# Optimization experiments

Measured on AMD Instinct MI355X. Metric: run time of the kernel, lower is better.

The kernel has to match this reference:

```python
import jax, jax.numpy as jnp
import numpy as np

LN_EPS = 1e-5


def setup_inputs() -> dict:
    key = jax.random.key(0)
    ks = jax.random.split(key, 8)
    dim = 256
    b, n3 = 8, 6144  # seq dim holds 3 concatenated token streams of n=2048 each
    s = 0.02
    return {
        "x": jax.random.normal(ks[0], (b, n3, dim), jnp.float32),
        "ln_g": jnp.ones((dim,), jnp.float32),
        "ln_b": jnp.zeros((dim,), jnp.float32),
        "Wq": jax.random.normal(ks[1], (dim, dim), jnp.float32) * s,
        "bq": jax.random.normal(ks[2], (dim,), jnp.float32) * s,
        "Wk": jax.random.normal(ks[3], (dim, dim), jnp.float32) * s,
        "bk": jax.random.normal(ks[4], (dim,), jnp.float32) * s,
        "Wv": jax.random.normal(ks[5], (dim, dim), jnp.float32) * s,
        "bv": jax.random.normal(ks[6], (dim,), jnp.float32) * s,
        "Wo": jax.random.normal(ks[7], (dim, dim), jnp.float32) * s,
        "bo": jnp.zeros((dim,), jnp.float32),
        "heads": 8,
    }


def reference(x, ln_g, ln_b, Wq, bq, Wk, bk, Wv, bv, Wo, bo, heads):
    dim = x.shape[-1]
    scale = dim ** (-0.5)  # NOTE: full dim, as in the original module
    d = dim // heads

    def cross_attn(xcat):
        # LayerNorm over last dim (applied to concatenated [2b, n, dim])
        mu = jnp.mean(xcat, axis=-1, keepdims=True)
        var = jnp.mean(jnp.square(xcat - mu), axis=-1, keepdims=True)
        xn = (xcat - mu) * jax.lax.rsqrt(var + LN_EPS) * ln_g + ln_b
        x1, x2 = jnp.split(xn, 2, axis=0)  # queries from stream 1, kv from stream 2
        q = x1 @ Wq.T + bq
        k = x2 @ Wk.T + bk
        v = x2 @ Wv.T + bv
        b_, n_ = q.shape[0], q.shape[1]
        q = q.reshape(b_, n_, heads, d).transpose(0, 2, 1, 3)  # b h n d
        k = k.reshape(b_, n_, heads, d).transpose(0, 2, 1, 3)
        v = v.reshape(b_, n_, heads, d).transpose(0, 2, 1, 3)
        dots = jnp.einsum('bhid,bhjd->bhij', q, k) * scale
        attn = jax.nn.softmax(dots, axis=-1)
        out = jnp.einsum('bhij,bhjd->bhid', attn, v)
        out = out.transpose(0, 2, 1, 3).reshape(b_, n_, dim)
        return out @ Wo.T + bo  # dropout is identity in eval

    x_origin, x_emap, x_lbp = jnp.split(x, 3, axis=1)
    out_oe = cross_attn(jnp.concatenate((x_origin, x_emap), axis=0))
    out_ol = cross_attn(jnp.concatenate((x_origin, x_lbp), axis=0))
    return out_oe + out_ol
```

## Files before the change

### kernel.cpp

```cpp
#include <hip/hip_runtime.h>
#include <hip/hip_bf16.h>
#include <math.h>

#define LN_EPS 1e-5f
#define QSCALE 0.09016844005556021f

typedef __attribute__((ext_vector_type(8))) short short8;
typedef __attribute__((ext_vector_type(4))) short short4v;
typedef __attribute__((ext_vector_type(4))) float f32x4;

__device__ inline ushort f2bf(float f) {
  __hip_bfloat16 h = __float2bfloat16(f);
  return *reinterpret_cast<ushort*>(&h);
}

__device__ inline uint pk2bf(float a, float b) {
  uint ua = __float_as_uint(a) + 0x8000u;
  uint ub = __float_as_uint(b) + 0x8000u;
  return __builtin_amdgcn_perm(ub, ua, 0x07060302u);
}


__global__ __launch_bounds__(256) void ln_wcast_kernel(
    const float* __restrict__ x, const float* __restrict__ lng,
    const float* __restrict__ lnb,
    const float* __restrict__ Wq, const float* __restrict__ Wk,
    const float* __restrict__ Wv, const float* __restrict__ Wo,
    ushort* __restrict__ xn, ushort* __restrict__ wbf) {
  if (blockIdx.x < 256) {
    int t = blockIdx.x * 256 + threadIdx.x;
    int e0 = t * 4;
    int m = e0 >> 16, off = e0 & 65535;
    const float* src = (m == 0) ? Wq : (m == 1) ? Wk : (m == 2) ? Wv : Wo;
    float4 v = *(const float4*)(src + off);
    ushort4 o;
    o.x = f2bf(v.x); o.y = f2bf(v.y); o.z = f2bf(v.z); o.w = f2bf(v.w);
    *(ushort4*)(wbf + m * 65536 + off) = o;
    return;
  }
  int w = threadIdx.x >> 6;
  int lane = threadIdx.x & 63;
  size_t token = (size_t)(blockIdx.x - 256) * 4 + w;
  float4 v = *(const float4*)(x + token * 256 + lane * 4);
  float s  = v.x + v.y + v.z + v.w;
  float s2 = v.x * v.x + v.y * v.y + v.z * v.z + v.w * v.w;
#pragma unroll
  for (int off = 32; off >= 1; off >>= 1) {
    s  += __shfl_xor(s, off, 64);
    s2 += __shfl_xor(s2, off, 64);
  }
  float mu  = s * (1.0f / 256.0f);
  float var = s2 * (1.0f / 256.0f) - mu * mu;
  float rs  = rsqrtf(var + LN_EPS);
  float4 g = *(const float4*)(lng + lane * 4);
  float4 bb = *(const float4*)(lnb + lane * 4);
  ushort4 o;
  o.x = f2bf((v.x - mu) * rs * g.x + bb.x);
  o.y = f2bf((v.y - mu) * rs * g.y + bb.y);
  o.z = f2bf((v.z - mu) * rs * g.z + bb.z);
  o.w = f2bf((v.w - mu) * rs * g.w + bb.w);
  *(ushort4*)(xn + token * 256 + lane * 4) = o;
}

__global__ __launch_bounds__(256) void proj_kernel(
    const ushort* __restrict__ xn,
    const ushort* __restrict__ wq, const ushort* __restrict__ wk,
    const ushort* __restrict__ wv,
    const float* __restrict__ bq, const float* __restrict__ bk,
    const float* __restrict__ bv,
    ushort* __restrict__ qb, ushort* __restrict__ keb, ushort* __restrict__ vTe,
    ushort* __restrict__ klb, ushort* __restrict__ vTl) {
  int z = blockIdx.z;
  int tid = threadIdx.x;
  int w = tid >> 6, lane = tid & 63;
  int n = lane & 15, quad = lane >> 4;
  int cbase = blockIdx.y * 128 + w * 32;
  int b = (blockIdx.x * 128) >> 11;
  int r0 = (blockIdx.x * 128) & 2047;

  if (z == 0) {
    const ushort* xbase = xn + ((size_t)b * 6144 + r0) * 256;
    short8 wf[2][8];
#pragma unroll
    for (int ct = 0; ct < 2; ++ct)
#pragma unroll
      for (int kc = 0; kc < 8; ++kc)
        wf[ct][kc] = *(const short8*)(wq + (size_t)(cbase + ct * 16 + n) * 256 + kc * 32 + quad * 8);
    float4 bt[2];
    bt[0] = *(const float4*)(bq + cbase + quad * 4);
    bt[1] = *(const float4*)(bq + cbase + 16 + quad * 4);

    short8 xfA[8], xfB[8];
#pragma unroll
    for (int kc = 0; kc < 8; ++kc)
      xfA[kc] = *(const short8*)(xbase + (size_t)n * 256 + kc * 32 + quad * 8);

#pragma unroll
    for (int tt = 0; tt < 8; ++tt) {
      const short8* cur = (tt & 1) ? xfB : xfA;
      short8* nxt = (tt & 1) ? xfA : xfB;
      if (tt < 7) {
#pragma unroll
        for (int kc = 0; kc < 8; ++kc)
          nxt[kc] = *(const short8*)(xbase + (size_t)((tt + 1) * 16 + n) * 256 + kc * 32 + quad * 8);
      }
      f32x4 acc[2] = {{0.f, 0.f, 0.f, 0.f}, {0.f, 0.f, 0.f, 0.f}};
#pragma unroll
      for (int ct = 0; ct < 2; ++ct)
#pragma unroll
        for (int kc = 0; kc < 8; ++kc)
          acc[ct] = __builtin_amdgcn_mfma_f32_16x16x32_bf16(wf[ct][kc], cur[kc], acc[ct], 0, 0, 0);
      int n2 = r0 + tt * 16 + n;
#pragma unroll
      for (int ct = 0; ct < 2; ++ct) {
        int c = cbase + ct * 16 + quad * 4;
        int h = c >> 5, d = c & 31;
        float* bp = (float*)&bt[ct];
        ushort4 st;
        st.x = f2bf((acc[ct][0] + bp[0]) * QSCALE);
        st.y = f2bf((acc[ct][1] + bp[1]) * QSCALE);
        st.z = f2bf((acc[ct][2] + bp[2]) * QSCALE);
        st.w = f2bf((acc[ct][3] + bp[3]) * QSCALE);
        *(ushort4*)(qb + (((size_t)(b * 8 + h) * 2048) + n2) * 32 + d) = st;
      }
    }
  } else {
    int s = z;
    ushort* kout = (z == 1) ? keb : klb;
    ushort* vout = (z == 1) ? vTe : vTl;
    const ushort* xbase = xn + ((size_t)b * 6144 + s * 2048 + r0) * 256;
    short8 wfk[2][8], wfv[2][8];
#pragma unroll
    for (int ct = 0; ct < 2; ++ct)
#pragma unroll
      for (int kc = 0; kc < 8; ++kc) {
        wfk[ct][kc] = *(const short8*)(wk + (size_t)(cbase + ct * 16 + n) * 256 + kc * 32 + quad * 8);
        wfv[ct][kc] = *(const short8*)(wv + (size_t)(cbase + ct * 16 + n) * 256 + kc * 32 + quad * 8);
      }
    float4 btk[2];
    btk[0] = *(const float4*)(bk + cbase + quad * 4);
    btk[1] = *(const float4*)(bk + cbase + 16 + quad * 4);
    float bsv[2] = {bv[cbase + n], bv[cbase + 16 + n]};

    short8 xfA[8], xfB[8];
#pragma unroll
    for (int kc = 0; kc < 8; ++kc)
      xfA[kc] = *(const short8*)(xbase + (size_t)n * 256 + kc * 32 + quad * 8);

#pragma unroll
    for (int tt = 0; tt < 8; ++tt) {
      const short8* cur = (tt & 1) ? xfB : xfA;
      short8* nxt = (tt & 1) ? xfA : xfB;
      if (tt < 7) {
#pragma unroll
        for (int kc = 0; kc < 8; ++kc)
          nxt[kc] = *(const short8*)(xbase + (size_t)((tt + 1) * 16 + n) * 256 + kc * 32 + quad * 8);
      }
      f32x4 ack[2] = {{0.f, 0.f, 0.f, 0.f}, {0.f, 0.f, 0.f, 0.f}};
      f32x4 acv[2] = {{0.f, 0.f, 0.f, 0.f}, {0.f, 0.f, 0.f, 0.f}};
#pragma unroll
      for (int ct = 0; ct < 2; ++ct)
#pragma unroll
        for (int kc = 0; kc < 8; ++kc) {
          ack[ct] = __builtin_amdgcn_mfma_f32_16x16x32_bf16(wfk[ct][kc], cur[kc], ack[ct], 0, 0, 0);
          acv[ct] = __builtin_amdgcn_mfma_f32_16x16x32_bf16(cur[kc], wfv[ct][kc], acv[ct], 0, 0, 0);
        }
      int n2 = r0 + tt * 16 + n;
#pragma unroll
      for (int ct = 0; ct < 2; ++ct) {
        int c = cbase + ct * 16 + quad * 4;
        int h = c >> 5, d = c & 31;
        float* bp = (float*)&btk[ct];
        ushort4 st;
        st.x = f2bf(ack[ct][0] + bp[0]);
        st.y = f2bf(ack[ct][1] + bp[1]);
        st.z = f2bf(ack[ct][2] + bp[2]);
        st.w = f2bf(ack[ct][3] + bp[3]);
        *(ushort4*)(kout + (((size_t)(b * 8 + h) * 2048) + n2) * 32 + d) = st;
      }
      int tq = r0 + tt * 16 + quad * 4;
      int tile = tq >> 6;
      int t4 = (tq >> 4) & 3;
      int qp = (tq >> 2) & 3;
#pragma unroll
      for (int ct = 0; ct < 2; ++ct) {
        int c = cbase + ct * 16 + n;
        int h = c >> 5, d = c & 31;
        int dh = d >> 4, np = d & 15;
        ushort4 st;
        st.x = f2bf(acv[ct][0] + bsv[ct]);
        st.y = f2bf(acv[ct][1] + bsv[ct]);
        st.z = f2bf(acv[ct][2] + bsv[ct]);
        st.w = f2bf(acv[ct][3] + bsv[ct]);
        *(ushort4*)(vout + (size_t)(b * 8 + h) * 65536
                    + (size_t)((((tile * 2 + dh) * 4 + t4) * 64 + qp * 16 + np) * 4)) = st;
      }
    }
  }
}

__global__ __launch_bounds__(256, 3) void attn_kernel(
    const ushort* __restrict__ q,
    const ushort* __restrict__ ke, const ushort* __restrict__ vTe,
    const ushort* __restrict__ kl, const ushort* __restrict__ vTl,
    ushort* __restrict__ osum) {
  int tid = threadIdx.x;
  int w = tid >> 6, lane = tid & 63;
  int n = lane & 15, quad = lane >> 4;

  union { uint2 u; short4v s; } one_u;
  one_u.u.x = 0x3F803F80u; one_u.u.y = 0x3F803F80u;
  const short4v vone = one_u.s;

  int L = blockIdx.y * 8 + blockIdx.x;
  int xcd = L & 7, idx = L >> 3;
  int bh = (idx & 7) * 8 + xcd;
  int q0 = (idx >> 3) * 128;
  int qbase = q0 + w * 32;

  short8 qfrag[2];
#pragma unroll
  for (int gq = 0; gq < 2; ++gq)
    qfrag[gq] = *(const short8*)(q + ((size_t)bh * 2048 + qbase + gq * 16 + n) * 32 + quad * 8);

  f32x4 outv[2][2];
#pragma unroll
  for (int gq = 0; gq < 2; ++gq)
#pragma unroll
    for (int dh = 0; dh < 2; ++dh) outv[gq][dh] = (f32x4){0.f, 0.f, 0.f, 0.f};

  for (int s = 0; s < 2; ++s) {
    const ushort* K  = (s == 0 ? ke : kl) + (size_t)bh * 2048 * 32;
    const ushort* VT = (s == 0 ? vTe : vTl) + (size_t)bh * 65536;
    f32x4 lacc[2];
    f32x4 oacc[2][2];
#pragma unroll
    for (int gq = 0; gq < 2; ++gq) {
      lacc[gq] = (f32x4){0.f, 0.f, 0.f, 0.f};
#pragma unroll
      for (int dh = 0; dh < 2; ++dh) oacc[gq][dh] = (f32x4){0.f, 0.f, 0.f, 0.f};
    }

    short8 kfc[4], kfn[4];
    short4v vfc[2][4], vfn[2][4];
#pragma unroll
    for (int t4 = 0; t4 < 4; ++t4)
      kfc[t4] = *(const short8*)(K + (size_t)(t4 * 16 + n) * 32 + quad * 8);
#pragma unroll
    for (int dh = 0; dh < 2; ++dh)
#pragma unroll
      for (int t4 = 0; t4 < 4; ++t4)
        vfc[dh][t4] = *(const short4v*)(VT + (dh * 4 + t4) * 256 + lane * 4);

    for (int jt = 0; jt < 32; ++jt) {
      if (jt < 31) {
        size_t tb = (size_t)(jt + 1) * 2048;
#pragma unroll
        for (int t4 = 0; t4 < 4; ++t4)
          kfn[t4] = *(const short8*)(K + tb + (size_t)(t4 * 16 + n) * 32 + quad * 8);
#pragma unroll
        for (int dh = 0; dh < 2; ++dh)
#pragma unroll
          for (int t4 = 0; t4 < 4; ++t4)
            vfn[dh][t4] = *(const short4v*)(VT + tb + (dh * 4 + t4) * 256 + lane * 4);
      }
#pragma unroll
      for (int gq = 0; gq < 2; ++gq) {
        f32x4 sacc[4];
#pragma unroll
        for (int t4 = 0; t4 < 4; ++t4) {
          f32x4 z = {0.f, 0.f, 0.f, 0.f};
          sacc[t4] = __builtin_amdgcn_mfma_f32_16x16x32_bf16(kfc[t4], qfrag[gq], z, 0, 0, 0);
        }
        short4v pf[4];
#pragma unroll
        for (int t4 = 0; t4 < 4; ++t4) {
          float p0 = __builtin_amdgcn_exp2f(sacc[t4][0]);
          float p1 = __builtin_amdgcn_exp2f(sacc[t4][1]);
          float p2 = __builtin_amdgcn_exp2f(sacc[t4][2]);
          float p3 = __builtin_amdgcn_exp2f(sacc[t4][3]);
          union { uint2 u; short4v s4; } cv;
          cv.u.x = pk2bf(p0, p1);
          cv.u.y = pk2bf(p2, p3);
          pf[t4] = cv.s4;
        }
#pragma unroll
        for (int t4 = 0; t4 < 4; ++t4) {
          oacc[gq][0] = __builtin_amdgcn_mfma_f32_16x16x16bf16_1k(
              pf[t4], vfc[0][t4], oacc[gq][0], 0, 0, 0);
          oacc[gq][1] = __builtin_amdgcn_mfma_f32_16x16x16bf16_1k(
              pf[t4], vfc[1][t4], oacc[gq][1], 0, 0, 0);
          lacc[gq] = __builtin_amdgcn_mfma_f32_16x16x16bf16_1k(
              pf[t4], vone, lacc[gq], 0, 0, 0);
        }
      }
#pragma unroll
      for (int t4 = 0; t4 < 4; ++t4) kfc[t4] = kfn[t4];
#pragma unroll
      for (int dh = 0; dh < 2; ++dh)
#pragma unroll
        for (int t4 = 0; t4 < 4; ++t4) vfc[dh][t4] = vfn[dh][t4];
    }
#pragma unroll
    for (int gq = 0; gq < 2; ++gq) {
      f32x4 inv;
#pragma unroll
      for (int r = 0; r < 4; ++r) inv[r] = __builtin_amdgcn_rcpf(lacc[gq][r]);
#pragma unroll
      for (int dh = 0; dh < 2; ++dh)
        outv[gq][dh] += oacc[gq][dh] * inv;
    }
  }

  int b = bh >> 3, h = bh & 7;
#pragma unroll
  for (int gq = 0; gq < 2; ++gq)
#pragma unroll
    for (int dh = 0; dh < 2; ++dh) {
      f32x4 v = outv[gq][dh];
#pragma unroll
      for (int r = 0; r < 4; ++r) {
        size_t row = (size_t)b * 2048 + qbase + gq * 16 + quad * 4 + r;
        osum[row * 256 + h * 32 + dh * 16 + n] = f2bf(v[r]);
      }
    }
}

__global__ __launch_bounds__(256) void outproj_kernel(
    const ushort* __restrict__ osum, const ushort* __restrict__ wo,
    const float* __restrict__ bo, float* __restrict__ out) {
  int tid = threadIdx.x;
  int w = tid >> 6, lane = tid & 63;
  int n = lane & 15, quad = lane >> 4;
  int cbase = blockIdx.y * 128 + w * 32;

  short8 wfrag[2][8];
#pragma unroll
  for (int ct = 0; ct < 2; ++ct)
#pragma unroll
    for (int kc = 0; kc < 8; ++kc)
      wfrag[ct][kc] = *(const short8*)(wo + (size_t)(cbase + ct * 16 + n) * 256 + kc * 32 + quad * 8);
  float4 bt[2];
  bt[0] = *(const float4*)(bo + cbase + quad * 4);
  bt[1] = *(const float4*)(bo + cbase + 16 + quad * 4);

  const ushort* abase = osum + (size_t)(blockIdx.x * 128) * 256;
  short8 xfA[8], xfB[8];
#pragma unroll
  for (int kc = 0; kc < 8; ++kc)
    xfA[kc] = *(const short8*)(abase + (size_t)n * 256 + kc * 32 + quad * 8);

#pragma unroll
  for (int tt = 0; tt < 8; ++tt) {
    const short8* cur = (tt & 1) ? xfB : xfA;
    short8* nxt = (tt & 1) ? xfA : xfB;
    if (tt < 7) {
#pragma unroll
      for (int kc = 0; kc < 8; ++kc)
        nxt[kc] = *(const short8*)(abase + (size_t)((tt + 1) * 16 + n) * 256 + kc * 32 + quad * 8);
    }
    int tok = blockIdx.x * 128 + tt * 16 + n;
    f32x4 acc[2] = {{0.f, 0.f, 0.f, 0.f}, {0.f, 0.f, 0.f, 0.f}};
#pragma unroll
    for (int ct = 0; ct < 2; ++ct)
#pragma unroll
      for (int kc = 0; kc < 8; ++kc)
        acc[ct] = __builtin_amdgcn_mfma_f32_16x16x32_bf16(wfrag[ct][kc], cur[kc], acc[ct], 0, 0, 0);
#pragma unroll
    for (int ct = 0; ct < 2; ++ct) {
      int c = cbase + ct * 16 + quad * 4;
      float* bp = (float*)&bt[ct];
      float4 st;
      st.x = acc[ct][0] + 2.0f * bp[0];
      st.y = acc[ct][1] + 2.0f * bp[1];
      st.z = acc[ct][2] + 2.0f * bp[2];
      st.w = acc[ct][3] + 2.0f * bp[3];
      *(float4*)(out + (size_t)tok * 256 + c) = st;
    }
  }
}

extern "C" void kernel_launch(void* const* d_in, const int* in_sizes, int n_in,
                              void* d_out, int out_size, void* d_ws, size_t ws_size,
                              hipStream_t stream) {
  const float* x   = (const float*)d_in[0];
  const float* lng = (const float*)d_in[1];
  const float* lnb = (const float*)d_in[2];
  const float* Wq  = (const float*)d_in[3];
  const float* bq  = (const float*)d_in[4];
  const float* Wk  = (const float*)d_in[5];
  const float* bk  = (const float*)d_in[6];
  const float* Wv  = (const float*)d_in[7];
  const float* bv  = (const float*)d_in[8];
  const float* Wo  = (const float*)d_in[9];
  const float* bo  = (const float*)d_in[10];
  float* out = (float*)d_out;

  ushort* ws = (ushort*)d_ws;
  const size_t XN  = (size_t)49152 * 256;
  const size_t QKV = (size_t)64 * 2048 * 32;
  ushort* xn   = ws;
  ushort* wbf  = xn + XN;
  ushort* qb   = wbf + 4 * 65536;
  ushort* keb  = qb  + QKV;
  ushort* vTe  = keb + QKV;
  ushort* klb  = vTe + QKV;
  ushort* vTl  = klb + QKV;
  ushort* osum = vTl + QKV;

  hipLaunchKernelGGL(ln_wcast_kernel, dim3(12544), dim3(256), 0, stream,
                     x, lng, lnb, Wq, Wk, Wv, Wo, xn, wbf);
  hipLaunchKernelGGL(proj_kernel, dim3(128, 2, 3), dim3(256), 0, stream,
                     xn, wbf, wbf + 65536, wbf + 131072, bq, bk, bv,
                     qb, keb, vTe, klb, vTl);
  hipLaunchKernelGGL(attn_kernel, dim3(8, 128), dim3(256), 0, stream,
                     qb, keb, vTe, klb, vTl, osum);
  hipLaunchKernelGGL(outproj_kernel, dim3(128, 2), dim3(256), 0, stream,
                     osum, wbf + 196608, bo, out);
}
```

Before: 290.8 us.

## Shrink attention per-wave query tile to 16 rows and drop K/V prefetch

Each wave in the attention kernel now handles 16 query rows instead of 32, so the grid doubles to 2048 blocks. The register double-buffering of the next K/V tile is removed and the block-to-(batch,head,query) mapping is reordered so consecutive blocks share a head. The launch-bounds occupancy hint is dropped. The aim is lower register pressure and more resident waves to hide load latency, at the cost of loading K/V twice as often per query row and losing software prefetch.

```diff
diff --git a/kernel.cpp b/kernel.cpp
--- a/kernel.cpp
+++ b/kernel.cpp
@@ -199,7 +199,7 @@
   }
 }
 
-__global__ __launch_bounds__(256, 3) void attn_kernel(
+__global__ __launch_bounds__(256) void attn_kernel(
     const ushort* __restrict__ q,
     const ushort* __restrict__ ke, const ushort* __restrict__ vTe,
     const ushort* __restrict__ kl, const ushort* __restrict__ vTl,
@@ -214,116 +214,79 @@
 
   int L = blockIdx.y * 8 + blockIdx.x;
   int xcd = L & 7, idx = L >> 3;
-  int bh = (idx & 7) * 8 + xcd;
-  int q0 = (idx >> 3) * 128;
-  int qbase = q0 + w * 32;
-
-  short8 qfrag[2];
-#pragma unroll
-  for (int gq = 0; gq < 2; ++gq)
-    qfrag[gq] = *(const short8*)(q + ((size_t)bh * 2048 + qbase + gq * 16 + n) * 32 + quad * 8);
-
-  f32x4 outv[2][2];
-#pragma unroll
-  for (int gq = 0; gq < 2; ++gq)
-#pragma unroll
-    for (int dh = 0; dh < 2; ++dh) outv[gq][dh] = (f32x4){0.f, 0.f, 0.f, 0.f};
+  int bh = xcd + 8 * (idx >> 5);
+  int q0 = (idx & 31) * 64;
+  int qbase = q0 + w * 16;
+
+  short8 qfrag = *(const short8*)(q + ((size_t)bh * 2048 + qbase + n) * 32 + quad * 8);
+
+  f32x4 outv[2];
+  outv[0] = (f32x4){0.f, 0.f, 0.f, 0.f};
+  outv[1] = (f32x4){0.f, 0.f, 0.f, 0.f};
 
   for (int s = 0; s < 2; ++s) {
     const ushort* K  = (s == 0 ? ke : kl) + (size_t)bh * 2048 * 32;
     const ushort* VT = (s == 0 ? vTe : vTl) + (size_t)bh * 65536;
-    f32x4 lacc[2];
-    f32x4 oacc[2][2];
-#pragma unroll
-    for (int gq = 0; gq < 2; ++gq) {
-      lacc[gq] = (f32x4){0.f, 0.f, 0.f, 0.f};
-#pragma unroll
-      for (int dh = 0; dh < 2; ++dh) oacc[gq][dh] = (f32x4){0.f, 0.f, 0.f, 0.f};
-    }
-
-    short8 kfc[4], kfn[4];
-    short4v vfc[2][4], vfn[2][4];
-#pragma unroll
-    for (int t4 = 0; t4 < 4; ++t4)
-      kfc[t4] = *(const short8*)(K + (size_t)(t4 * 16 + n) * 32 + quad * 8);
-#pragma unroll
-    for (int dh = 0; dh < 2; ++dh)
+    f32x4 lacc = (f32x4){0.f, 0.f, 0.f, 0.f};
+    f32x4 oacc[2];
+    oacc[0] = (f32x4){0.f, 0.f, 0.f, 0.f};
+    oacc[1] = (f32x4){0.f, 0.f, 0.f, 0.f};
+
+    for (int jt = 0; jt < 32; ++jt) {
+      size_t tb = (size_t)jt * 2048;
+      short8 kf[4];
 #pragma unroll
       for (int t4 = 0; t4 < 4; ++t4)
-        vfc[dh][t4] = *(const short4v*)(VT + (dh * 4 + t4) * 256 + lane * 4);
-
-    for (int jt = 0; jt < 32; ++jt) {
-      if (jt < 31) {
-        size_t tb = (size_t)(jt + 1) * 2048;
+        kf[t4] = *(const short8*)(K + tb + (size_t)(t4 * 16 + n) * 32 + quad * 8);
+      short4v vf[2][4];
+#pragma unroll
+      for (int dh = 0; dh < 2; ++dh)
 #pragma unroll
         for (int t4 = 0; t4 < 4; ++t4)
-          kfn[t4] = *(const short8*)(K + tb + (size_t)(t4 * 16 + n) * 32 + quad * 8);
-#pragma unroll
-        for (int dh = 0; dh < 2; ++dh)
-#pragma unroll
-          for (int t4 = 0; t4 < 4; ++t4)
-            vfn[dh][t4] = *(const short4v*)(VT + tb + (dh * 4 + t4) * 256 + lane * 4);
-      }
-#pragma unroll
-      for (int gq = 0; gq < 2; ++gq) {
-        f32x4 sacc[4];
-#pragma unroll
-        for (int t4 = 0; t4 < 4; ++t4) {
-          f32x4 z = {0.f, 0.f, 0.f, 0.f};
-          sacc[t4] = __builtin_amdgcn_mfma_f32_16x16x32_bf16(kfc[t4], qfrag[gq], z, 0, 0, 0);
-        }
-        short4v pf[4];
-#pragma unroll
-        for (int t4 = 0; t4 < 4; ++t4) {
-          float p0 = __builtin_amdgcn_exp2f(sacc[t4][0]);
-          float p1 = __builtin_amdgcn_exp2f(sacc[t4][1]);
-          float p2 = __builtin_amdgcn_exp2f(sacc[t4][2]);
-          float p3 = __builtin_amdgcn_exp2f(sacc[t4][3]);
-          union { uint2 u; short4v s4; } cv;
-          cv.u.x = pk2bf(p0, p1);
-          cv.u.y = pk2bf(p2, p3);
-          pf[t4] = cv.s4;
-        }
-#pragma unroll
-        for (int t4 = 0; t4 < 4; ++t4) {
-          oacc[gq][0] = __builtin_amdgcn_mfma_f32_16x16x16bf16_1k(
-              pf[t4], vfc[0][t4], oacc[gq][0], 0, 0, 0);
-          oacc[gq][1] = __builtin_amdgcn_mfma_f32_16x16x16bf16_1k(
-              pf[t4], vfc[1][t4], oacc[gq][1], 0, 0, 0);
-          lacc[gq] = __builtin_amdgcn_mfma_f32_16x16x16bf16_1k(
-              pf[t4], vone, lacc[gq], 0, 0, 0);
-        }
-      }
-#pragma unroll
-      for (int t4 = 0; t4 < 4; ++t4) kfc[t4] = kfn[t4];
-#pragma unroll
-      for (int dh = 0; dh < 2; ++dh)
-#pragma unroll
-        for (int t4 = 0; t4 < 4; ++t4) vfc[dh][t4] = vfn[dh][t4];
-    }
-#pragma unroll
-    for (int gq = 0; gq < 2; ++gq) {
-      f32x4 inv;
-#pragma unroll
-      for (int r = 0; r < 4; ++r) inv[r] = __builtin_amdgcn_rcpf(lacc[gq][r]);
-#pragma unroll
-      for (int dh = 0; dh < 2; ++dh)
-        outv[gq][dh] += oacc[gq][dh] * inv;
-    }
+          vf[dh][t4] = *(const short4v*)(VT + tb + (dh * 4 + t4) * 256 + lane * 4);
+
+      f32x4 sacc[4];
+#pragma unroll
+      for (int t4 = 0; t4 < 4; ++t4) {
+        f32x4 z = {0.f, 0.f, 0.f, 0.f};
+        sacc[t4] = __builtin_amdgcn_mfma_f32_16x16x32_bf16(kf[t4], qfrag, z, 0, 0, 0);
+      }
+      short4v pf[4];
+#pragma unroll
+      for (int t4 = 0; t4 < 4; ++t4) {
+        float p0 = __builtin_amdgcn_exp2f(sacc[t4][0]);
+        float p1 = __builtin_amdgcn_exp2f(sacc[t4][1]);
+        float p2 = __builtin_amdgcn_exp2f(sacc[t4][2]);
+        float p3 = __builtin_amdgcn_exp2f(sacc[t4][3]);
+        union { uint2 u; short4v s4; } cv;
+        cv.u.x = pk2bf(p0, p1);
+        cv.u.y = pk2bf(p2, p3);
+        pf[t4] = cv.s4;
+      }
+#pragma unroll
+      for (int t4 = 0; t4 < 4; ++t4) {
+        oacc[0] = __builtin_amdgcn_mfma_f32_16x16x16bf16_1k(pf[t4], vf[0][t4], oacc[0], 0, 0, 0);
+        oacc[1] = __builtin_amdgcn_mfma_f32_16x16x16bf16_1k(pf[t4], vf[1][t4], oacc[1], 0, 0, 0);
+        lacc    = __builtin_amdgcn_mfma_f32_16x16x16bf16_1k(pf[t4], vone, lacc, 0, 0, 0);
+      }
+    }
+    f32x4 inv;
+#pragma unroll
+    for (int r = 0; r < 4; ++r) inv[r] = __builtin_amdgcn_rcpf(lacc[r]);
+    outv[0] += oacc[0] * inv;
+    outv[1] += oacc[1] * inv;
   }
 
   int b = bh >> 3, h = bh & 7;
 #pragma unroll
-  for (int gq = 0; gq < 2; ++gq)
-#pragma unroll
-    for (int dh = 0; dh < 2; ++dh) {
-      f32x4 v = outv[gq][dh];
-#pragma unroll
-      for (int r = 0; r < 4; ++r) {
-        size_t row = (size_t)b * 2048 + qbase + gq * 16 + quad * 4 + r;
-        osum[row * 256 + h * 32 + dh * 16 + n] = f2bf(v[r]);
-      }
-    }
+  for (int dh = 0; dh < 2; ++dh) {
+    f32x4 v = outv[dh];
+#pragma unroll
+    for (int r = 0; r < 4; ++r) {
+      size_t row = (size_t)b * 2048 + qbase + quad * 4 + r;
+      osum[row * 256 + h * 32 + dh * 16 + n] = f2bf(v[r]);
+    }
+  }
 }
 
 __global__ __launch_bounds__(256) void outproj_kernel(
@@ -413,7 +376,7 @@
   hipLaunchKernelGGL(proj_kernel, dim3(128, 2, 3), dim3(256), 0, stream,
                      xn, wbf, wbf + 65536, wbf + 131072, bq, bk, bv,
                      qb, keb, vTe, klb, vTl);
-  hipLaunchKernelGGL(attn_kernel, dim3(8, 128), dim3(256), 0, stream,
+  hipLaunchKernelGGL(attn_kernel, dim3(8, 256), dim3(256), 0, stream,
                      qb, keb, vTe, klb, vTl, osum);
   hipLaunchKernelGGL(outproj_kernel, dim3(128, 2), dim3(256), 0, stream,
                      osum, wbf + 196608, bo, out);
```

Result: slower. 394.1 us (+35.5%).
